# Optimization experiments

Measured on AMD Instinct MI355X. Metric: run time of the kernel, lower is better.

## Reference

```python
import jax, jax.numpy as jnp
import numpy as np

N = 131072       # total nodes (B graphs x P nodes)
P = 4096         # nodes per graph
B = 32           # graphs in batch
E = 2097152      # edges (avg degree 16)
IN_DIM = 64
HID = 128
OUT = 16
EPS = 1e-5
SLOPE = 0.01


def _degrees(idx):
    # structural degree, clamped to min 1 (as DGL GraphConv does)
    d = jax.ops.segment_sum(jnp.ones((E,), jnp.float32), idx, num_segments=N)
    return jnp.maximum(d, 1.0)


def _graph_conv(x, W, src, dst, ew):
    # DGL GraphConv, norm='both', bias=False, with scalar edge weights:
    # h = D_out^{-1/2} x ; m_v = sum_{(u->v)} w_e h_u ; out = (D_in^{-1/2} m) W
    h = x * jax.lax.rsqrt(_degrees(src))[:, None]
    m = jax.ops.segment_sum(ew[:, None] * h[src], dst, num_segments=N)  # [N, F]
    return (m * jax.lax.rsqrt(_degrees(dst))[:, None]) @ W


def _graph_norm(x, gamma, beta, alpha):
    # GraphNorm (Cai et al. / PyG, batch=None): stats over all nodes per feature
    mu = jnp.mean(x, axis=0)
    c = x - alpha * mu
    var = jnp.mean(c * c, axis=0)
    return c * jax.lax.rsqrt(var + EPS) * gamma + beta


def _mean_nodes(h, gid):
    # per-graph mean readout; every graph has exactly P nodes
    return jax.ops.segment_sum(h, gid, num_segments=B) / P


def setup_inputs() -> dict:
    key = jax.random.key(0)
    ks = jax.random.split(key, 8)
    src = jax.random.randint(ks[0], (E,), 0, N, dtype=jnp.int32)
    # keep edges within each 4096-node graph block (batched DGL graph)
    dst = (src // P) * P + jax.random.randint(ks[1], (E,), 0, P, dtype=jnp.int32)
    features = jax.random.normal(ks[2], (N, IN_DIM), jnp.float32)
    edge_weights = jax.random.uniform(ks[3], (E,), jnp.float32)
    # kaiming/xavier-scale init approximations
    W1 = jax.random.normal(ks[4], (IN_DIM, HID), jnp.float32) * np.sqrt(2.0 / IN_DIM)
    W2 = jax.random.normal(ks[5], (HID, HID), jnp.float32) * np.sqrt(2.0 / HID)
    Wc = jax.random.normal(ks[6], (OUT, 2 * HID), jnp.float32) * np.sqrt(1.0 / (2 * HID))
    ones = jnp.ones((HID,), jnp.float32)
    zeros = jnp.zeros((HID,), jnp.float32)
    return {
        'features': features, 'edge_weights': edge_weights, 'src': src, 'dst': dst,
        'W1': W1, 'W2': W2, 'Wc': Wc,
        'gamma1': ones, 'beta1': zeros, 'alpha1': ones,
        'gamma2': ones, 'beta2': zeros, 'alpha2': ones,
    }


def reference(features, edge_weights, src, dst, W1, W2, Wc,
              gamma1, beta1, alpha1, gamma2, beta2, alpha2):
    gid = jnp.arange(N, dtype=jnp.int32) // P  # node -> graph id
    h1 = _graph_conv(features, W1, src, dst, edge_weights)
    h1 = jax.nn.leaky_relu(_graph_norm(h1, gamma1, beta1, alpha1), SLOPE)
    r1 = _mean_nodes(h1, gid)                  # [B, HID]
    h2 = _graph_conv(h1, W2, src, dst, edge_weights)
    h2 = jax.nn.leaky_relu(_graph_norm(h2, gamma2, beta2, alpha2), SLOPE)
    r2 = _mean_nodes(h2, gid)                  # [B, HID]
    readouts = jnp.concatenate([r1, r2], axis=1)  # [B, 2*HID]
    return readouts @ Wc.T                     # [B, OUT]
```

## Files before the change

### kernel.cpp

```cpp
#include <hip/hip_runtime.h>
#include <hip/hip_fp16.h>

constexpr int NN   = 131072;
constexpr int PP   = 4096;
constexpr int BG   = 32;
constexpr int EE   = 2097152;
constexpr int IND  = 64;
constexpr int HH   = 128;
constexpr int CAP  = 81920;
constexpr float EPSV   = 1e-5f;
constexpr float SLOPEV = 0.01f;

typedef short bf16x8 __attribute__((ext_vector_type(8)));
typedef float f32x4  __attribute__((ext_vector_type(4)));
typedef float f32x2  __attribute__((ext_vector_type(2)));

__device__ __forceinline__ unsigned f2bf(float f) {
    unsigned u = __float_as_uint(f);
    return (u + 0x7FFFu + ((u >> 16) & 1u)) >> 16;
}
__device__ __forceinline__ unsigned pack2bf(float lo, float hi) {
    return f2bf(lo) | (f2bf(hi) << 16);
}
__device__ __forceinline__ float bflo(unsigned p) { return __uint_as_float(p << 16); }
__device__ __forceinline__ float bfhi(unsigned p) { return __uint_as_float(p & 0xFFFF0000u); }
__device__ __forceinline__ float w16(unsigned r) {
    return __half2float(__ushort_as_half((unsigned short)(r >> 16)));
}

template <int K>
__device__ __forceinline__ void packw_body(const float* __restrict__ W,
                                           unsigned short* __restrict__ pw, int t) {
    if (t >= K * 16) return;
    int lane = t & 63, nt = (t >> 6) & 7, kt = t >> 9;
    int kbase = kt * 32 + ((lane >> 4) & 3) * 8;
    int col   = nt * 16 + (lane & 15);
    for (int j = 0; j < 8; j++)
        pw[t * 8 + j] = (unsigned short)f2bf(W[(kbase + j) * HH + col]);
}

__global__ __launch_bounds__(256) void k_prep(const float* __restrict__ features,
                                              unsigned* __restrict__ f8x,
                                              const float* __restrict__ W1,
                                              unsigned short* __restrict__ pw1,
                                              const float* __restrict__ W2,
                                              unsigned short* __restrict__ pw2,
                                              int* __restrict__ gcur,
                                              float* __restrict__ racc,
                                              unsigned* __restrict__ csr2) {
    int b = blockIdx.x, t = threadIdx.x;
    if (b < 8192) {
        int i = b * 256 + t;
        float4 v = ((const float4*)features)[i];
        int w0 = __builtin_amdgcn_cvt_pk_fp8_f32(v.x, v.y, 0, false);
        int w1 = __builtin_amdgcn_cvt_pk_fp8_f32(v.z, v.w, w0, true);
        f8x[i] = (unsigned)w1;
        return;
    }
    if (b == 8192) {
        if (t < BG) gcur[t * 16] = t * CAP;
        for (int i = t; i < 2 * BG * HH; i += 256) racc[i] = 0.f;
        return;
    }
    if (b < 8197) { packw_body<64>(W1, pw1, (b - 8193) * 256 + t); return; }
    if (b < 8205) { packw_body<128>(W2, pw2, (b - 8197) * 256 + t); return; }
    ((uint4*)csr2)[(b - 8205) * 256 + t] = make_uint4(0, 0, 0, 0);
}

__global__ __launch_bounds__(256) void k_part(const int* __restrict__ src,
                                              const int* __restrict__ dst,
                                              const float* __restrict__ ew,
                                              int* __restrict__ gcur,
                                              uint2* __restrict__ recs) {
    __shared__ int cnt[32];
    __shared__ int start[32];
    __shared__ int gbase[32];
    __shared__ uint2 stage[4096];
    int t = threadIdx.x;
    int ebase = blockIdx.x * 4096;
    if (t < 32) cnt[t] = 0;
    __syncthreads();
    int es[16]; int ed[16]; float ev[16];
#pragma unroll
    for (int k = 0; k < 16; k++) {
        int e = ebase + k * 256 + t;
        es[k] = src[e]; ed[k] = dst[e]; ev[k] = ew[e];
        atomicAdd(&cnt[es[k] >> 12], 1);
    }
    __syncthreads();
    if (t == 0) {
        int run = 0;
        for (int g = 0; g < 32; g++) { start[g] = run; run += cnt[g]; }
    }
    __syncthreads();
    if (t < 32) {
        gbase[t] = atomicAdd(&gcur[t * 16], cnt[t]);
        cnt[t] = start[t];
    }
    __syncthreads();
#pragma unroll
    for (int k = 0; k < 16; k++) {
        int g = es[k] >> 12;
        int pos = atomicAdd(&cnt[g], 1);
        stage[pos] = make_uint2((unsigned)(es[k] & 4095) | ((unsigned)(ed[k] & 4095) << 12) |
                                ((unsigned)g << 24), __float_as_uint(ev[k]));
    }
    __syncthreads();
    for (int i = t; i < 4096; i += 256) {
        uint2 r = stage[i];
        int g = r.x >> 24;
        recs[gbase[g] + (i - start[g])] = r;
    }
}

__global__ __launch_bounds__(1024) void k_hist(const uint2* __restrict__ recs,
                                               const int* __restrict__ gcur,
                                               int* __restrict__ shist,
                                               int* __restrict__ dhist) {
    __shared__ int hs[4096];
    __shared__ int hd[4096];
    int t = threadIdx.x;
    int g = blockIdx.x >> 3, c = blockIdx.x & 7;
    int n = gcur[g * 16] - g * CAP;
    int lo = (n * c) >> 3, hi = (n * (c + 1)) >> 3;
    ((int4*)hs)[t] = make_int4(0, 0, 0, 0);
    ((int4*)hd)[t] = make_int4(0, 0, 0, 0);
    __syncthreads();
    const uint2* base = recs + (size_t)g * CAP;
    for (int i = lo + t; i < hi; i += 1024) {
        unsigned x = base[i].x;
        atomicAdd(&hs[x & 4095], 1);
        atomicAdd(&hd[(x >> 12) & 4095], 1);
    }
    __syncthreads();
    ((int4*)(shist + (size_t)blockIdx.x * 4096))[t] = ((int4*)hs)[t];
    ((int4*)(dhist + (size_t)blockIdx.x * 4096))[t] = ((int4*)hd)[t];
}

__global__ __launch_bounds__(1024) void k_offs(int* __restrict__ shist,
                                               int* __restrict__ dhist,
                                               float* __restrict__ rs_s,
                                               float* __restrict__ rsd,
                                               int* __restrict__ degd,
                                               int* __restrict__ offs) {
    __shared__ int partial[1024];
    int t = threadIdx.x, g = blockIdx.x;
    int sdeg[4] = {0, 0, 0, 0}, ddeg[4] = {0, 0, 0, 0};
#pragma unroll
    for (int c = 0; c < 8; c++) {
        int4 sv = ((const int4*)(shist + (size_t)(g * 8 + c) * 4096))[t];
        int4 dv = ((const int4*)(dhist + (size_t)(g * 8 + c) * 4096))[t];
        sdeg[0] += sv.x; sdeg[1] += sv.y; sdeg[2] += sv.z; sdeg[3] += sv.w;
        ddeg[0] += dv.x; ddeg[1] += dv.y; ddeg[2] += dv.z; ddeg[3] += dv.w;
    }
    int pdeg[4];
#pragma unroll
    for (int j = 0; j < 4; j++) {
        int idx = t * 4 + j;
        int vs = sdeg[j]; if (vs < 1) vs = 1;
        rs_s[g * PP + idx] = rsqrtf((float)vs);
        int vd = ddeg[j]; if (vd < 1) vd = 1;
        rsd[g * PP + idx]  = rsqrtf((float)vd);
        pdeg[j] = (ddeg[j] + 3) & ~3;
        degd[g * PP + idx] = pdeg[j];
    }
    partial[t] = pdeg[0] + pdeg[1] + pdeg[2] + pdeg[3];
    __syncthreads();
    for (int off = 1; off < 1024; off <<= 1) {
        int v = partial[t];
        int add = (t >= off) ? partial[t - off] : 0;
        __syncthreads();
        partial[t] = v + add;
        __syncthreads();
    }
    int run = (t == 0) ? 0 : partial[t - 1];
#pragma unroll
    for (int j = 0; j < 4; j++) {
        int idx = t * 4 + j;
        offs[g * PP + idx] = g * CAP + run;
        int nb = run;
        for (int c = 0; c < 8; c++) {
            size_t hidx = (size_t)(g * 8 + c) * 4096 + idx;
            int v = dhist[hidx];
            dhist[hidx] = nb;
            nb += v;
        }
        run += pdeg[j];
    }
}

__global__ __launch_bounds__(1024) void k_place(const uint2* __restrict__ recs,
                                                const int* __restrict__ gcur,
                                                const int* __restrict__ dhist,
                                                const float* __restrict__ rs_s,
                                                unsigned* __restrict__ csr2) {
    __shared__ int cur[4096];
    __shared__ float rss[4096];
    int t = threadIdx.x;
    int g = blockIdx.x >> 3, c = blockIdx.x & 7;
    int n = gcur[g * 16] - g * CAP;
    int lo = (n * c) >> 3, hi = (n * (c + 1)) >> 3;
    ((int4*)cur)[t] = ((const int4*)(dhist + (size_t)blockIdx.x * 4096))[t];
    ((float4*)rss)[t] = ((const float4*)(rs_s + (size_t)g * PP))[t];
    __syncthreads();
    const uint2* base = recs + (size_t)g * CAP;
    unsigned* cbase = csr2 + (size_t)g * CAP;
    for (int i = lo + t; i < hi; i += 1024) {
        uint2 r = base[i];
        int sl = r.x & 4095, dl = (r.x >> 12) & 4095;
        int pos = atomicAdd(&cur[dl], 1);
        float wf = __uint_as_float(r.y) * rss[sl];
        cbase[pos] = (unsigned)sl | ((unsigned)__half_as_ushort(__float2half(wf)) << 16);
    }
}

__device__ __forceinline__ void eacc2(unsigned rec, uint2 q,
                                      f32x2& P01, f32x2& P23, f32x2& P45, f32x2& P67) {
    f32x2 l0 = __builtin_amdgcn_cvt_pk_f32_fp8((int)q.x, false);
    f32x2 h0 = __builtin_amdgcn_cvt_pk_f32_fp8((int)q.x, true);
    f32x2 l1 = __builtin_amdgcn_cvt_pk_f32_fp8((int)q.y, false);
    f32x2 h1 = __builtin_amdgcn_cvt_pk_f32_fp8((int)q.y, true);
    float w = w16(rec);
    P01 += l0 * w; P23 += h0 * w; P45 += l1 * w; P67 += h1 * w;
}

template <int RW2>
__device__ __forceinline__ void agg_dual_w(const uint2* __restrict__ hp,
                                           const unsigned* __restrict__ csr2,
                                           int oa, int ca, int ob, int cb,
                                           f32x2& A01, f32x2& A23, f32x2& A45, f32x2& A67,
                                           f32x2& B01, f32x2& B23, f32x2& B45, f32x2& B67) {
    f32x2 z = {0.f, 0.f};
    A01 = z; A23 = z; A45 = z; A67 = z;
    B01 = z; B23 = z; B45 = z; B67 = z;
    int c0 = ca < cb ? ca : cb;
    int cm = ca < cb ? cb : ca;
    int i = 0;
    for (; i < c0; i += 4) {
        uint4 ra = *(const uint4*)(csr2 + oa + i);
        uint4 rb = *(const uint4*)(csr2 + ob + i);
        uint2 qa0 = hp[(ra.x & 4095u) * RW2];
        uint2 qa1 = hp[(ra.y & 4095u) * RW2];
        uint2 qa2 = hp[(ra.z & 4095u) * RW2];
        uint2 qa3 = hp[(ra.w & 4095u) * RW2];
        uint2 qb0 = hp[(rb.x & 4095u) * RW2];
        uint2 qb1 = hp[(rb.y & 4095u) * RW2];
        uint2 qb2 = hp[(rb.z & 4095u) * RW2];
        uint2 qb3 = hp[(rb.w & 4095u) * RW2];
        eacc2(ra.x, qa0, A01, A23, A45, A67);
        eacc2(ra.y, qa1, A01, A23, A45, A67);
        eacc2(ra.z, qa2, A01, A23, A45, A67);
        eacc2(ra.w, qa3, A01, A23, A45, A67);
        eacc2(rb.x, qb0, B01, B23, B45, B67);
        eacc2(rb.y, qb1, B01, B23, B45, B67);
        eacc2(rb.z, qb2, B01, B23, B45, B67);
        eacc2(rb.w, qb3, B01, B23, B45, B67);
    }
    if (i < cm) {
        int ot = (ca > cb) ? oa : ob;
        f32x2 E01 = z, E23 = z, E45 = z, E67 = z;
        for (; i < cm; i += 4) {
            uint4 rr = *(const uint4*)(csr2 + ot + i);
            uint2 q0 = hp[(rr.x & 4095u) * RW2];
            uint2 q1 = hp[(rr.y & 4095u) * RW2];
            uint2 q2 = hp[(rr.z & 4095u) * RW2];
            uint2 q3 = hp[(rr.w & 4095u) * RW2];
            eacc2(rr.x, q0, E01, E23, E45, E67);
            eacc2(rr.y, q1, E01, E23, E45, E67);
            eacc2(rr.z, q2, E01, E23, E45, E67);
            eacc2(rr.w, q3, E01, E23, E45, E67);
        }
        if (ca > cb) { A01 += E01; A23 += E23; A45 += E45; A67 += E67; }
        else         { B01 += E01; B23 += E23; B45 += E45; B67 += E67; }
    }
}

__global__ __launch_bounds__(256) void k_aggemm1(const unsigned* __restrict__ f8x,
                                                 const unsigned* __restrict__ csr2,
                                                 const int* __restrict__ offs,
                                                 const int* __restrict__ degd,
                                                 const float* __restrict__ rsd,
                                                 const short* __restrict__ PW,
                                                 unsigned short* __restrict__ C,
                                                 float* __restrict__ part) {
    constexpr int WP = 36;
    __shared__ unsigned lds[64 * WP];
    __shared__ float s1[HH], s2[HH];
    int t = threadIdx.x;
    if (t < HH) { s1[t] = 0.f; s2[t] = 0.f; }
    int bid = blockIdx.x;
    int xcd = bid & 7, idx = bid >> 3;
    int g = xcd * 4 + (idx >> 6);
    int node0 = g * PP + (idx & 63) * 64;
    int lane = t & 63, wv = t >> 6;
    int grp = lane >> 3, gl = lane & 7;
    const uint2* hp = (const uint2*)f8x + (size_t)((unsigned)(g * PP)) * 8 + gl;
    {
        int lrA = wv * 16 + grp * 2;
        int va = node0 + lrA;
        int2 oo = *(const int2*)(offs + va);
        int2 dd = *(const int2*)(degd + va);
        f32x2 A01, A23, A45, A67, B01, B23, B45, B67;
        agg_dual_w<8>(hp, csr2, oo.x, dd.x, oo.y, dd.y,
                      A01, A23, A45, A67, B01, B23, B45, B67);
        float2 rr2 = *(const float2*)(rsd + va);
        *(uint4*)&lds[lrA * WP + gl * 4] = make_uint4(
            pack2bf(A01.x * rr2.x, A01.y * rr2.x), pack2bf(A23.x * rr2.x, A23.y * rr2.x),
            pack2bf(A45.x * rr2.x, A45.y * rr2.x), pack2bf(A67.x * rr2.x, A67.y * rr2.x));
        *(uint4*)&lds[(lrA + 1) * WP + gl * 4] = make_uint4(
            pack2bf(B01.x * rr2.y, B01.y * rr2.y), pack2bf(B23.x * rr2.y, B23.y * rr2.y),
            pack2bf(B45.x * rr2.y, B45.y * rr2.y), pack2bf(B67.x * rr2.y, B67.y * rr2.y));
    }
    __syncthreads();
    int m = lane & 15, quad = lane >> 4;
    bf16x8 a[2];
#pragma unroll
    for (int kt = 0; kt < 2; kt++)
        a[kt] = *(const bf16x8*)&lds[(wv * 16 + m) * WP + kt * 16 + quad * 4];
#pragma unroll
    for (int nt = 0; nt < 8; nt++) {
        f32x4 acc = {0.f, 0.f, 0.f, 0.f};
#pragma unroll
        for (int kt = 0; kt < 2; kt++) {
            bf16x8 b = *(const bf16x8*)(PW + ((size_t)(kt * 8 + nt) * 64 + lane) * 8);
            acc = __builtin_amdgcn_mfma_f32_16x16x32_bf16(a[kt], b, acc, 0, 0, 0);
        }
        int col = nt * 16 + m;
        int r0 = node0 + wv * 16 + quad * 4;
        float ps = 0.f, pq = 0.f;
#pragma unroll
        for (int r = 0; r < 4; r++) {
            C[(size_t)(r0 + r) * HH + col] = (unsigned short)f2bf(acc[r]);
            ps += acc[r]; pq += acc[r] * acc[r];
        }
        atomicAdd(&s1[col], ps);
        atomicAdd(&s2[col], pq);
    }
    __syncthreads();
    if (t < HH) {
        part[bid * 256 + t]      = s1[t];
        part[bid * 256 + HH + t] = s2[t];
    }
}

__global__ __launch_bounds__(256) void k_aggemm2(const unsigned* __restrict__ f8,
                                                 const unsigned* __restrict__ csr2,
                                                 const int* __restrict__ offs,
                                                 const int* __restrict__ degd,
                                                 const float* __restrict__ rsd,
                                                 const short* __restrict__ PW,
                                                 unsigned short* __restrict__ C,
                                                 float* __restrict__ part) {
    constexpr int WP = 68;
    __shared__ unsigned lds[64 * WP];
    __shared__ float s1[HH], s2[HH];
    int t = threadIdx.x;
    if (t < HH) { s1[t] = 0.f; s2[t] = 0.f; }
    int bid = blockIdx.x;
    int xcd = bid & 7, idx = bid >> 3;
    int g = xcd * 4 + (idx >> 6);
    int node0 = g * PP + (idx & 63) * 64;
    int lane = t & 63, wv = t >> 6;
    int grp = lane >> 4, gl = lane & 15;
    const uint2* hp = (const uint2*)f8 + (size_t)((unsigned)(g * PP)) * 16 + gl;
    for (int p = 0; p < 2; p++) {
        int lrA = wv * 16 + p * 8 + grp * 2;
        int va = node0 + lrA;
        int2 oo = *(const int2*)(offs + va);
        int2 dd = *(const int2*)(degd + va);
        f32x2 A01, A23, A45, A67, B01, B23, B45, B67;
        agg_dual_w<16>(hp, csr2, oo.x, dd.x, oo.y, dd.y,
                       A01, A23, A45, A67, B01, B23, B45, B67);
        float2 rr2 = *(const float2*)(rsd + va);
        *(uint4*)&lds[lrA * WP + gl * 4] = make_uint4(
            pack2bf(A01.x * rr2.x, A01.y * rr2.x), pack2bf(A23.x * rr2.x, A23.y * rr2.x),
            pack2bf(A45.x * rr2.x, A45.y * rr2.x), pack2bf(A67.x * rr2.x, A67.y * rr2.x));
        *(uint4*)&lds[(lrA + 1) * WP + gl * 4] = make_uint4(
            pack2bf(B01.x * rr2.y, B01.y * rr2.y), pack2bf(B23.x * rr2.y, B23.y * rr2.y),
            pack2bf(B45.x * rr2.y, B45.y * rr2.y), pack2bf(B67.x * rr2.y, B67.y * rr2.y));
    }
    __syncthreads();
    int m = lane & 15, quad = lane >> 4;
    bf16x8 a[4];
#pragma unroll
    for (int kt = 0; kt < 4; kt++)
        a[kt] = *(const bf16x8*)&lds[(wv * 16 + m) * WP + kt * 16 + quad * 4];
#pragma unroll
    for (int nt = 0; nt < 8; nt++) {
        f32x4 acc = {0.f, 0.f, 0.f, 0.f};
#pragma unroll
        for (int kt = 0; kt < 4; kt++) {
            bf16x8 b = *(const bf16x8*)(PW + ((size_t)(kt * 8 + nt) * 64 + lane) * 8);
            acc = __builtin_amdgcn_mfma_f32_16x16x32_bf16(a[kt], b, acc, 0, 0, 0);
        }
        int col = nt * 16 + m;
        int r0 = node0 + wv * 16 + quad * 4;
        float ps = 0.f, pq = 0.f;
#pragma unroll
        for (int r = 0; r < 4; r++) {
            C[(size_t)(r0 + r) * HH + col] = (unsigned short)f2bf(acc[r]);
            ps += acc[r]; pq += acc[r] * acc[r];
        }
        atomicAdd(&s1[col], ps);
        atomicAdd(&s2[col], pq);
    }
    __syncthreads();
    if (t < HH) {
        part[bid * 256 + t]      = s1[t];
        part[bid * 256 + HH + t] = s2[t];
    }
}

__global__ __launch_bounds__(256) void k_red(const float* __restrict__ part,
                                             float* __restrict__ pb) {
    int t = threadIdx.x, b = blockIdx.x;
    float s = 0.f;
    for (int r = 0; r < 32; r++) s += part[(size_t)(b * 32 + r) * 256 + t];
    pb[b * 256 + t] = s;
}

__global__ void k_coef(const float* __restrict__ pb, const float* __restrict__ gamma,
                       const float* __restrict__ beta, const float* __restrict__ alpha,
                       float* __restrict__ ab) {
    int t = threadIdx.x;
    float s = 0.f;
    for (int b = 0; b < 64; b++) s += pb[b * 256 + t];
    __shared__ float sh[256];
    sh[t] = s;
    __syncthreads();
    if (t < 128) {
        float mu = sh[t] * (1.f / NN);
        float e2 = sh[128 + t] * (1.f / NN);
        float al = alpha[t];
        float var = e2 - (2.f * al - al * al) * mu * mu;
        float a = rsqrtf(var + EPSV) * gamma[t];
        ab[t] = a;
        ab[HH + t] = beta[t] - al * mu * a;
    }
}

template <bool WRITE>
__global__ __launch_bounds__(256) void k_normro(const unsigned* __restrict__ h,
                                                const float* __restrict__ ab,
                                                float* __restrict__ racc,
                                                unsigned short* __restrict__ f8) {
    int fp = threadIdx.x & 63;
    int q  = threadIdx.x >> 6;
    int node0 = blockIdx.x * 64;
    int g = node0 / PP;
    float a0 = ab[2 * fp], a1 = ab[2 * fp + 1];
    float b0 = ab[HH + 2 * fp], b1 = ab[HH + 2 * fp + 1];
    float s0 = 0.f, s1 = 0.f;
    for (int i = q; i < 64; i += 4) {
        size_t idx = (size_t)(node0 + i) * 64 + fp;
        unsigned v = h[idx];
        float x0 = fmaf(a0, bflo(v), b0); x0 = x0 > 0.f ? x0 : SLOPEV * x0;
        float x1 = fmaf(a1, bfhi(v), b1); x1 = x1 > 0.f ? x1 : SLOPEV * x1;
        if (WRITE) f8[idx] = (unsigned short)__builtin_amdgcn_cvt_pk_fp8_f32(x0, x1, 0, false);
        s0 += x0; s1 += x1;
    }
    __shared__ float sh[512];
    sh[threadIdx.x] = s0;
    sh[256 + threadIdx.x] = s1;
    __syncthreads();
    if (q == 0) {
        float t0 = s0 + sh[64 + fp] + sh[128 + fp] + sh[192 + fp];
        float t1 = s1 + sh[256 + 64 + fp] + sh[256 + 128 + fp] + sh[256 + 192 + fp];
        atomicAdd(&racc[g * HH + 2 * fp],     t0);
        atomicAdd(&racc[g * HH + 2 * fp + 1], t1);
    }
}

__global__ void k_final(const float* __restrict__ racc1, const float* __restrict__ racc2,
                        const float* __restrict__ Wc, float* __restrict__ out) {
    int t = threadIdx.x;
    int b = t >> 4, o = t & 15;
    float acc = 0.f;
    for (int f = 0; f < HH; f++) acc += racc1[b * HH + f] * Wc[o * (2 * HH) + f];
    for (int f = 0; f < HH; f++) acc += racc2[b * HH + f] * Wc[o * (2 * HH) + HH + f];
    out[t] = acc * (1.f / PP);
}

extern "C" void kernel_launch(void* const* d_in, const int* in_sizes, int n_in,
                              void* d_out, int out_size, void* d_ws, size_t ws_size,
                              hipStream_t stream) {
    const float* features = (const float*)d_in[0];
    const float* ew       = (const float*)d_in[1];
    const int*   src      = (const int*)d_in[2];
    const int*   dst      = (const int*)d_in[3];
    const float* W1       = (const float*)d_in[4];
    const float* W2       = (const float*)d_in[5];
    const float* Wc       = (const float*)d_in[6];
    const float* gamma1   = (const float*)d_in[7];
    const float* beta1    = (const float*)d_in[8];
    const float* alpha1   = (const float*)d_in[9];
    const float* gamma2   = (const float*)d_in[10];
    const float* beta2    = (const float*)d_in[11];
    const float* alpha2   = (const float*)d_in[12];
    float* out = (float*)d_out;

    char* w = (char*)d_ws;
    int*    gcur   = (int*)(w + 0);
    float*  racc1  = (float*)(w + (16u << 10));
    float*  racc2  = (float*)(w + (32u << 10));
    float*  ab1    = (float*)(w + (48u << 10));
    float*  ab2    = (float*)(w + (52u << 10));
    unsigned short* pw1 = (unsigned short*)(w + (64u << 10));
    unsigned short* pw2 = (unsigned short*)(w + (80u << 10));
    float*  pb     = (float*)(w + (128u << 10));
    float*  rs_s   = (float*)(w + (1024u << 10));
    float*  rsd    = (float*)(w + (1536u << 10));
    int*    degd   = (int*)(w + (2048u << 10));
    int*    offs   = (int*)(w + (2560u << 10));
    float*  part   = (float*)(w + (3u << 20));
    int*    shist  = (int*)(w + (5u << 20));
    int*    dhist  = (int*)(w + (9u << 20));
    unsigned* csr2 = (unsigned*)(w + (13u << 20));
    unsigned* mbuf = (unsigned*)(w + (23u << 20));
    unsigned* hbuf = (unsigned*)(w + (55u << 20));
    uint2*    recs = (uint2*)(w + (87u << 20));
    unsigned* f8x  = (unsigned*)(w + (107u << 20));
    unsigned* f8buf= (unsigned*)(w + (123u << 20));

    k_prep<<<10765, 256, 0, stream>>>(features, f8x, W1, pw1, W2, pw2, gcur, racc1, csr2);

    k_part<<<EE / 4096, 256, 0, stream>>>(src, dst, ew, gcur, recs);
    k_hist<<<BG * 8, 1024, 0, stream>>>(recs, gcur, shist, dhist);
    k_offs<<<BG, 1024, 0, stream>>>(shist, dhist, rs_s, rsd, degd, offs);
    k_place<<<BG * 8, 1024, 0, stream>>>(recs, gcur, dhist, rs_s, csr2);

    k_aggemm1<<<NN / 64, 256, 0, stream>>>(f8x, csr2, offs, degd, rsd,
                                           (const short*)pw1, (unsigned short*)hbuf, part);
    k_red<<<64, 256, 0, stream>>>(part, pb);
    k_coef<<<1, 256, 0, stream>>>(pb, gamma1, beta1, alpha1, ab1);
    k_normro<true><<<NN / 64, 256, 0, stream>>>(hbuf, ab1, racc1, (unsigned short*)f8buf);

    k_aggemm2<<<NN / 64, 256, 0, stream>>>(f8buf, csr2, offs, degd, rsd,
                                           (const short*)pw2, (unsigned short*)mbuf, part);
    k_red<<<64, 256, 0, stream>>>(part, pb);
    k_coef<<<1, 256, 0, stream>>>(pb, gamma2, beta2, alpha2, ab2);
    k_normro<false><<<NN / 64, 256, 0, stream>>>(mbuf, ab2, racc2, nullptr);

    k_final<<<1, 512, 0, stream>>>(racc1, racc2, Wc, out);
}
```

Measured before the change: 358.9 us.

## Build CSR directly with global atomics, dropping graph-partition and histogram passes

Replaces the four-kernel CSR build (partition edges by graph into records, per-chunk LDS histograms, scan, LDS-cursor placement) with three kernels. Degrees now come from global atomics straight off src/dst, a per-graph scan produces offsets and cursors, and edges are placed using global atomics on those cursors. This removes the intermediate record buffer and one full pass over edges, but it moves all counting and cursor atomics from LDS to global memory. The rs_s gather is also now random. The workspace zeroing grows to clear the new degree arrays.

```diff
diff --git a/kernel.cpp b/kernel.cpp
--- a/kernel.cpp
+++ b/kernel.cpp
@@ -45,7 +45,7 @@
                                               unsigned short* __restrict__ pw1,
                                               const float* __restrict__ W2,
                                               unsigned short* __restrict__ pw2,
-                                              int* __restrict__ gcur,
+                                              int* __restrict__ degz,
                                               float* __restrict__ racc,
                                               unsigned* __restrict__ csr2) {
     int b = blockIdx.x, t = threadIdx.x;
@@ -58,111 +58,58 @@
         return;
     }
     if (b == 8192) {
-        if (t < BG) gcur[t * 16] = t * CAP;
         for (int i = t; i < 2 * BG * HH; i += 256) racc[i] = 0.f;
         return;
     }
     if (b < 8197) { packw_body<64>(W1, pw1, (b - 8193) * 256 + t); return; }
     if (b < 8205) { packw_body<128>(W2, pw2, (b - 8197) * 256 + t); return; }
-    ((uint4*)csr2)[(b - 8205) * 256 + t] = make_uint4(0, 0, 0, 0);
-}
-
-__global__ __launch_bounds__(256) void k_part(const int* __restrict__ src,
-                                              const int* __restrict__ dst,
-                                              const float* __restrict__ ew,
-                                              int* __restrict__ gcur,
-                                              uint2* __restrict__ recs) {
-    __shared__ int cnt[32];
-    __shared__ int start[32];
-    __shared__ int gbase[32];
-    __shared__ uint2 stage[4096];
-    int t = threadIdx.x;
-    int ebase = blockIdx.x * 4096;
-    if (t < 32) cnt[t] = 0;
-    __syncthreads();
-    int es[16]; int ed[16]; float ev[16];
-#pragma unroll
-    for (int k = 0; k < 16; k++) {
-        int e = ebase + k * 256 + t;
-        es[k] = src[e]; ed[k] = dst[e]; ev[k] = ew[e];
-        atomicAdd(&cnt[es[k] >> 12], 1);
-    }
-    __syncthreads();
-    if (t == 0) {
-        int run = 0;
-        for (int g = 0; g < 32; g++) { start[g] = run; run += cnt[g]; }
-    }
-    __syncthreads();
-    if (t < 32) {
-        gbase[t] = atomicAdd(&gcur[t * 16], cnt[t]);
-        cnt[t] = start[t];
-    }
-    __syncthreads();
-#pragma unroll
-    for (int k = 0; k < 16; k++) {
-        int g = es[k] >> 12;
-        int pos = atomicAdd(&cnt[g], 1);
-        stage[pos] = make_uint2((unsigned)(es[k] & 4095) | ((unsigned)(ed[k] & 4095) << 12) |
-                                ((unsigned)g << 24), __float_as_uint(ev[k]));
-    }
-    __syncthreads();
-    for (int i = t; i < 4096; i += 256) {
-        uint2 r = stage[i];
-        int g = r.x >> 24;
-        recs[gbase[g] + (i - start[g])] = r;
-    }
-}
-
-__global__ __launch_bounds__(1024) void k_hist(const uint2* __restrict__ recs,
-                                               const int* __restrict__ gcur,
-                                               int* __restrict__ shist,
-                                               int* __restrict__ dhist) {
-    __shared__ int hs[4096];
-    __shared__ int hd[4096];
-    int t = threadIdx.x;
-    int g = blockIdx.x >> 3, c = blockIdx.x & 7;
-    int n = gcur[g * 16] - g * CAP;
-    int lo = (n * c) >> 3, hi = (n * (c + 1)) >> 3;
-    ((int4*)hs)[t] = make_int4(0, 0, 0, 0);
-    ((int4*)hd)[t] = make_int4(0, 0, 0, 0);
-    __syncthreads();
-    const uint2* base = recs + (size_t)g * CAP;
-    for (int i = lo + t; i < hi; i += 1024) {
-        unsigned x = base[i].x;
-        atomicAdd(&hs[x & 4095], 1);
-        atomicAdd(&hd[(x >> 12) & 4095], 1);
-    }
-    __syncthreads();
-    ((int4*)(shist + (size_t)blockIdx.x * 4096))[t] = ((int4*)hs)[t];
-    ((int4*)(dhist + (size_t)blockIdx.x * 4096))[t] = ((int4*)hd)[t];
-}
-
-__global__ __launch_bounds__(1024) void k_offs(int* __restrict__ shist,
-                                               int* __restrict__ dhist,
+    if (b < 10765) {
+        ((uint4*)csr2)[(b - 8205) * 256 + t] = make_uint4(0, 0, 0, 0);
+        return;
+    }
+    ((uint4*)degz)[(b - 10765) * 256 + t] = make_uint4(0, 0, 0, 0);
+}
+
+__global__ __launch_bounds__(256) void k_deg(const int* __restrict__ src,
+                                             const int* __restrict__ dst,
+                                             int* __restrict__ sdeg,
+                                             int* __restrict__ ddeg) {
+    int e0 = blockIdx.x * 2048 + threadIdx.x * 8;
+    int4 sa = *(const int4*)(src + e0), sb = *(const int4*)(src + e0 + 4);
+    int4 da = *(const int4*)(dst + e0), db = *(const int4*)(dst + e0 + 4);
+    atomicAdd(&sdeg[sa.x], 1); atomicAdd(&sdeg[sa.y], 1);
+    atomicAdd(&sdeg[sa.z], 1); atomicAdd(&sdeg[sa.w], 1);
+    atomicAdd(&sdeg[sb.x], 1); atomicAdd(&sdeg[sb.y], 1);
+    atomicAdd(&sdeg[sb.z], 1); atomicAdd(&sdeg[sb.w], 1);
+    atomicAdd(&ddeg[da.x], 1); atomicAdd(&ddeg[da.y], 1);
+    atomicAdd(&ddeg[da.z], 1); atomicAdd(&ddeg[da.w], 1);
+    atomicAdd(&ddeg[db.x], 1); atomicAdd(&ddeg[db.y], 1);
+    atomicAdd(&ddeg[db.z], 1); atomicAdd(&ddeg[db.w], 1);
+}
+
+__global__ __launch_bounds__(1024) void k_scan(const int* __restrict__ sdeg,
+                                               const int* __restrict__ ddeg,
                                                float* __restrict__ rs_s,
                                                float* __restrict__ rsd,
                                                int* __restrict__ degd,
-                                               int* __restrict__ offs) {
+                                               int* __restrict__ offs,
+                                               int* __restrict__ cur) {
     __shared__ int partial[1024];
     int t = threadIdx.x, g = blockIdx.x;
-    int sdeg[4] = {0, 0, 0, 0}, ddeg[4] = {0, 0, 0, 0};
-#pragma unroll
-    for (int c = 0; c < 8; c++) {
-        int4 sv = ((const int4*)(shist + (size_t)(g * 8 + c) * 4096))[t];
-        int4 dv = ((const int4*)(dhist + (size_t)(g * 8 + c) * 4096))[t];
-        sdeg[0] += sv.x; sdeg[1] += sv.y; sdeg[2] += sv.z; sdeg[3] += sv.w;
-        ddeg[0] += dv.x; ddeg[1] += dv.y; ddeg[2] += dv.z; ddeg[3] += dv.w;
-    }
+    int base = g * PP + t * 4;
+    int4 sd = *(const int4*)(sdeg + base);
+    int4 dd = *(const int4*)(ddeg + base);
+    int s[4] = {sd.x, sd.y, sd.z, sd.w};
+    int d[4] = {dd.x, dd.y, dd.z, dd.w};
     int pdeg[4];
 #pragma unroll
     for (int j = 0; j < 4; j++) {
-        int idx = t * 4 + j;
-        int vs = sdeg[j]; if (vs < 1) vs = 1;
-        rs_s[g * PP + idx] = rsqrtf((float)vs);
-        int vd = ddeg[j]; if (vd < 1) vd = 1;
-        rsd[g * PP + idx]  = rsqrtf((float)vd);
-        pdeg[j] = (ddeg[j] + 3) & ~3;
-        degd[g * PP + idx] = pdeg[j];
+        int vs = s[j] < 1 ? 1 : s[j];
+        rs_s[base + j] = rsqrtf((float)vs);
+        int vd = d[j] < 1 ? 1 : d[j];
+        rsd[base + j] = rsqrtf((float)vd);
+        pdeg[j] = (d[j] + 3) & ~3;
+        degd[base + j] = pdeg[j];
     }
     partial[t] = pdeg[0] + pdeg[1] + pdeg[2] + pdeg[3];
     __syncthreads();
@@ -176,41 +123,31 @@
     int run = (t == 0) ? 0 : partial[t - 1];
 #pragma unroll
     for (int j = 0; j < 4; j++) {
-        int idx = t * 4 + j;
-        offs[g * PP + idx] = g * CAP + run;
-        int nb = run;
-        for (int c = 0; c < 8; c++) {
-            size_t hidx = (size_t)(g * 8 + c) * 4096 + idx;
-            int v = dhist[hidx];
-            dhist[hidx] = nb;
-            nb += v;
-        }
+        offs[base + j] = g * CAP + run;
+        cur[base + j]  = g * CAP + run;
         run += pdeg[j];
     }
 }
 
-__global__ __launch_bounds__(1024) void k_place(const uint2* __restrict__ recs,
-                                                const int* __restrict__ gcur,
-                                                const int* __restrict__ dhist,
+__global__ __launch_bounds__(256) void k_place2(const int* __restrict__ src,
+                                                const int* __restrict__ dst,
+                                                const float* __restrict__ ew,
                                                 const float* __restrict__ rs_s,
+                                                int* __restrict__ cur,
                                                 unsigned* __restrict__ csr2) {
-    __shared__ int cur[4096];
-    __shared__ float rss[4096];
-    int t = threadIdx.x;
-    int g = blockIdx.x >> 3, c = blockIdx.x & 7;
-    int n = gcur[g * 16] - g * CAP;
-    int lo = (n * c) >> 3, hi = (n * (c + 1)) >> 3;
-    ((int4*)cur)[t] = ((const int4*)(dhist + (size_t)blockIdx.x * 4096))[t];
-    ((float4*)rss)[t] = ((const float4*)(rs_s + (size_t)g * PP))[t];
-    __syncthreads();
-    const uint2* base = recs + (size_t)g * CAP;
-    unsigned* cbase = csr2 + (size_t)g * CAP;
-    for (int i = lo + t; i < hi; i += 1024) {
-        uint2 r = base[i];
-        int sl = r.x & 4095, dl = (r.x >> 12) & 4095;
-        int pos = atomicAdd(&cur[dl], 1);
-        float wf = __uint_as_float(r.y) * rss[sl];
-        cbase[pos] = (unsigned)sl | ((unsigned)__half_as_ushort(__float2half(wf)) << 16);
+    int e0 = blockIdx.x * 2048 + threadIdx.x * 8;
+    int4 sa = *(const int4*)(src + e0), sb = *(const int4*)(src + e0 + 4);
+    int4 da = *(const int4*)(dst + e0), db = *(const int4*)(dst + e0 + 4);
+    float4 wa = *(const float4*)(ew + e0), wb = *(const float4*)(ew + e0 + 4);
+    int ss[8] = {sa.x, sa.y, sa.z, sa.w, sb.x, sb.y, sb.z, sb.w};
+    int ds[8] = {da.x, da.y, da.z, da.w, db.x, db.y, db.z, db.w};
+    float ws[8] = {wa.x, wa.y, wa.z, wa.w, wb.x, wb.y, wb.z, wb.w};
+#pragma unroll
+    for (int k = 0; k < 8; k++) {
+        float wf = ws[k] * rs_s[ss[k]];
+        int pos = atomicAdd(&cur[ds[k]], 1);
+        csr2[pos] = (unsigned)(ss[k] & 4095) |
+                    ((unsigned)__half_as_ushort(__float2half(wf)) << 16);
     }
 }
 
@@ -500,7 +437,6 @@
     float* out = (float*)d_out;
 
     char* w = (char*)d_ws;
-    int*    gcur   = (int*)(w + 0);
     float*  racc1  = (float*)(w + (16u << 10));
     float*  racc2  = (float*)(w + (32u << 10));
     float*  ab1    = (float*)(w + (48u << 10));
@@ -513,21 +449,20 @@
     int*    degd   = (int*)(w + (2048u << 10));
     int*    offs   = (int*)(w + (2560u << 10));
     float*  part   = (float*)(w + (3u << 20));
-    int*    shist  = (int*)(w + (5u << 20));
-    int*    dhist  = (int*)(w + (9u << 20));
+    int*    sdeg   = (int*)(w + (5u << 20));
+    int*    ddeg   = (int*)(w + (5u << 20) + (512u << 10));
+    int*    cur    = (int*)(w + (9u << 20));
     unsigned* csr2 = (unsigned*)(w + (13u << 20));
     unsigned* mbuf = (unsigned*)(w + (23u << 20));
     unsigned* hbuf = (unsigned*)(w + (55u << 20));
-    uint2*    recs = (uint2*)(w + (87u << 20));
     unsigned* f8x  = (unsigned*)(w + (107u << 20));
     unsigned* f8buf= (unsigned*)(w + (123u << 20));
 
-    k_prep<<<10765, 256, 0, stream>>>(features, f8x, W1, pw1, W2, pw2, gcur, racc1, csr2);
-
-    k_part<<<EE / 4096, 256, 0, stream>>>(src, dst, ew, gcur, recs);
-    k_hist<<<BG * 8, 1024, 0, stream>>>(recs, gcur, shist, dhist);
-    k_offs<<<BG, 1024, 0, stream>>>(shist, dhist, rs_s, rsd, degd, offs);
-    k_place<<<BG * 8, 1024, 0, stream>>>(recs, gcur, dhist, rs_s, csr2);
+    k_prep<<<11021, 256, 0, stream>>>(features, f8x, W1, pw1, W2, pw2, sdeg, racc1, csr2);
+
+    k_deg<<<EE / 2048, 256, 0, stream>>>(src, dst, sdeg, ddeg);
+    k_scan<<<BG, 1024, 0, stream>>>(sdeg, ddeg, rs_s, rsd, degd, offs, cur);
+    k_place2<<<EE / 2048, 256, 0, stream>>>(src, dst, ew, rs_s, cur, csr2);
 
     k_aggemm1<<<NN / 64, 256, 0, stream>>>(f8x, csr2, offs, degd, rsd,
                                            (const short*)pw1, (unsigned short*)hbuf, part);
```

Measured after the change: 561.2 us. 1.56x slower.

## Double aggemm threads per node block and fuse stat reduction kernels

Applied to the files above, without the earlier changes.

Both aggregation+GEMM kernels move from 256 to 512 threads per block. In layer 1 each 8-lane group now handles a single node instead of two. In layer 2 the per-thread loop over two passes is removed. The MFMA stage splits its eight column tiles across two wave halves. Separately, the two-kernel stat reduction (k_red then k_coef) is merged into one kernel that uses a last-block atomic counter to compute the norm coefficients, saving a launch per layer. The cost is extra threadfence and atomic overhead, plus doubled per-block register and thread demand.

```diff
diff --git a/kernel.cpp b/kernel.cpp
--- a/kernel.cpp
+++ b/kernel.cpp
@@ -47,7 +47,8 @@
                                               unsigned short* __restrict__ pw2,
                                               int* __restrict__ gcur,
                                               float* __restrict__ racc,
-                                              unsigned* __restrict__ csr2) {
+                                              unsigned* __restrict__ csr2,
+                                              int* __restrict__ scnt) {
     int b = blockIdx.x, t = threadIdx.x;
     if (b < 8192) {
         int i = b * 256 + t;
@@ -59,6 +60,7 @@
     }
     if (b == 8192) {
         if (t < BG) gcur[t * 16] = t * CAP;
+        if (t == 0) scnt[0] = 0;
         for (int i = t; i < 2 * BG * HH; i += 256) racc[i] = 0.f;
         return;
     }
@@ -275,7 +277,27 @@
     }
 }
 
-__global__ __launch_bounds__(256) void k_aggemm1(const unsigned* __restrict__ f8x,
+template <int RW2>
+__device__ __forceinline__ void agg_single_w(const uint2* __restrict__ hp,
+                                             const unsigned* __restrict__ csr2,
+                                             int oa, int ca,
+                                             f32x2& A01, f32x2& A23, f32x2& A45, f32x2& A67) {
+    f32x2 z = {0.f, 0.f};
+    A01 = z; A23 = z; A45 = z; A67 = z;
+    for (int i = 0; i < ca; i += 4) {
+        uint4 ra = *(const uint4*)(csr2 + oa + i);
+        uint2 q0 = hp[(ra.x & 4095u) * RW2];
+        uint2 q1 = hp[(ra.y & 4095u) * RW2];
+        uint2 q2 = hp[(ra.z & 4095u) * RW2];
+        uint2 q3 = hp[(ra.w & 4095u) * RW2];
+        eacc2(ra.x, q0, A01, A23, A45, A67);
+        eacc2(ra.y, q1, A01, A23, A45, A67);
+        eacc2(ra.z, q2, A01, A23, A45, A67);
+        eacc2(ra.w, q3, A01, A23, A45, A67);
+    }
+}
+
+__global__ __launch_bounds__(512) void k_aggemm1(const unsigned* __restrict__ f8x,
                                                  const unsigned* __restrict__ csr2,
                                                  const int* __restrict__ offs,
                                                  const int* __restrict__ degd,
@@ -292,33 +314,29 @@
     int xcd = bid & 7, idx = bid >> 3;
     int g = xcd * 4 + (idx >> 6);
     int node0 = g * PP + (idx & 63) * 64;
-    int lane = t & 63, wv = t >> 6;
-    int grp = lane >> 3, gl = lane & 7;
+    int gr = t >> 3, gl = t & 7;
     const uint2* hp = (const uint2*)f8x + (size_t)((unsigned)(g * PP)) * 8 + gl;
     {
-        int lrA = wv * 16 + grp * 2;
-        int va = node0 + lrA;
-        int2 oo = *(const int2*)(offs + va);
-        int2 dd = *(const int2*)(degd + va);
-        f32x2 A01, A23, A45, A67, B01, B23, B45, B67;
-        agg_dual_w<8>(hp, csr2, oo.x, dd.x, oo.y, dd.y,
-                      A01, A23, A45, A67, B01, B23, B45, B67);
-        float2 rr2 = *(const float2*)(rsd + va);
-        *(uint4*)&lds[lrA * WP + gl * 4] = make_uint4(
-            pack2bf(A01.x * rr2.x, A01.y * rr2.x), pack2bf(A23.x * rr2.x, A23.y * rr2.x),
-            pack2bf(A45.x * rr2.x, A45.y * rr2.x), pack2bf(A67.x * rr2.x, A67.y * rr2.x));
-        *(uint4*)&lds[(lrA + 1) * WP + gl * 4] = make_uint4(
-            pack2bf(B01.x * rr2.y, B01.y * rr2.y), pack2bf(B23.x * rr2.y, B23.y * rr2.y),
-            pack2bf(B45.x * rr2.y, B45.y * rr2.y), pack2bf(B67.x * rr2.y, B67.y * rr2.y));
-    }
-    __syncthreads();
+        int va = node0 + gr;
+        int oa = offs[va], ca = degd[va];
+        f32x2 A01, A23, A45, A67;
+        agg_single_w<8>(hp, csr2, oa, ca, A01, A23, A45, A67);
+        float rda = rsd[va];
+        *(uint4*)&lds[gr * WP + gl * 4] = make_uint4(
+            pack2bf(A01.x * rda, A01.y * rda), pack2bf(A23.x * rda, A23.y * rda),
+            pack2bf(A45.x * rda, A45.y * rda), pack2bf(A67.x * rda, A67.y * rda));
+    }
+    __syncthreads();
+    int lane = t & 63, wv = t >> 6;
+    int rowblk = wv & 3, colh = wv >> 2;
     int m = lane & 15, quad = lane >> 4;
     bf16x8 a[2];
 #pragma unroll
     for (int kt = 0; kt < 2; kt++)
-        a[kt] = *(const bf16x8*)&lds[(wv * 16 + m) * WP + kt * 16 + quad * 4];
-#pragma unroll
-    for (int nt = 0; nt < 8; nt++) {
+        a[kt] = *(const bf16x8*)&lds[(rowblk * 16 + m) * WP + kt * 16 + quad * 4];
+#pragma unroll
+    for (int nq = 0; nq < 4; nq++) {
+        int nt = colh * 4 + nq;
         f32x4 acc = {0.f, 0.f, 0.f, 0.f};
 #pragma unroll
         for (int kt = 0; kt < 2; kt++) {
@@ -326,7 +344,7 @@
             acc = __builtin_amdgcn_mfma_f32_16x16x32_bf16(a[kt], b, acc, 0, 0, 0);
         }
         int col = nt * 16 + m;
-        int r0 = node0 + wv * 16 + quad * 4;
+        int r0 = node0 + rowblk * 16 + quad * 4;
         float ps = 0.f, pq = 0.f;
 #pragma unroll
         for (int r = 0; r < 4; r++) {
@@ -343,7 +361,7 @@
     }
 }
 
-__global__ __launch_bounds__(256) void k_aggemm2(const unsigned* __restrict__ f8,
+__global__ __launch_bounds__(512) void k_aggemm2(const unsigned* __restrict__ f8,
                                                  const unsigned* __restrict__ csr2,
                                                  const int* __restrict__ offs,
                                                  const int* __restrict__ degd,
@@ -360,11 +378,10 @@
     int xcd = bid & 7, idx = bid >> 3;
     int g = xcd * 4 + (idx >> 6);
     int node0 = g * PP + (idx & 63) * 64;
-    int lane = t & 63, wv = t >> 6;
-    int grp = lane >> 4, gl = lane & 15;
+    int gr = t >> 4, gl = t & 15;
     const uint2* hp = (const uint2*)f8 + (size_t)((unsigned)(g * PP)) * 16 + gl;
-    for (int p = 0; p < 2; p++) {
-        int lrA = wv * 16 + p * 8 + grp * 2;
+    {
+        int lrA = gr * 2;
         int va = node0 + lrA;
         int2 oo = *(const int2*)(offs + va);
         int2 dd = *(const int2*)(degd + va);
@@ -380,13 +397,16 @@
             pack2bf(B45.x * rr2.y, B45.y * rr2.y), pack2bf(B67.x * rr2.y, B67.y * rr2.y));
     }
     __syncthreads();
+    int lane = t & 63, wv = t >> 6;
+    int rowblk = wv & 3, colh = wv >> 2;
     int m = lane & 15, quad = lane >> 4;
     bf16x8 a[4];
 #pragma unroll
     for (int kt = 0; kt < 4; kt++)
-        a[kt] = *(const bf16x8*)&lds[(wv * 16 + m) * WP + kt * 16 + quad * 4];
-#pragma unroll
-    for (int nt = 0; nt < 8; nt++) {
+        a[kt] = *(const bf16x8*)&lds[(rowblk * 16 + m) * WP + kt * 16 + quad * 4];
+#pragma unroll
+    for (int nq = 0; nq < 4; nq++) {
+        int nt = colh * 4 + nq;
         f32x4 acc = {0.f, 0.f, 0.f, 0.f};
 #pragma unroll
         for (int kt = 0; kt < 4; kt++) {
@@ -394,7 +414,7 @@
             acc = __builtin_amdgcn_mfma_f32_16x16x32_bf16(a[kt], b, acc, 0, 0, 0);
         }
         int col = nt * 16 + m;
-        int r0 = node0 + wv * 16 + quad * 4;
+        int r0 = node0 + rowblk * 16 + quad * 4;
         float ps = 0.f, pq = 0.f;
 #pragma unroll
         for (int r = 0; r < 4; r++) {
@@ -411,22 +431,27 @@
     }
 }
 
-__global__ __launch_bounds__(256) void k_red(const float* __restrict__ part,
-                                             float* __restrict__ pb) {
+__global__ __launch_bounds__(256) void k_stat(const float* __restrict__ part,
+                                              const float* __restrict__ gamma,
+                                              const float* __restrict__ beta,
+                                              const float* __restrict__ alpha,
+                                              float* __restrict__ ab,
+                                              float* __restrict__ pb,
+                                              int* __restrict__ scnt) {
     int t = threadIdx.x, b = blockIdx.x;
     float s = 0.f;
     for (int r = 0; r < 32; r++) s += part[(size_t)(b * 32 + r) * 256 + t];
     pb[b * 256 + t] = s;
-}
-
-__global__ void k_coef(const float* __restrict__ pb, const float* __restrict__ gamma,
-                       const float* __restrict__ beta, const float* __restrict__ alpha,
-                       float* __restrict__ ab) {
-    int t = threadIdx.x;
-    float s = 0.f;
-    for (int b = 0; b < 64; b++) s += pb[b * 256 + t];
+    __threadfence();
+    __shared__ int isLast;
+    if (t == 0) isLast = (atomicAdd(scnt, 1) == 63) ? 1 : 0;
+    __syncthreads();
+    if (!isLast) return;
+    __threadfence();
+    float tot = 0.f;
+    for (int bb = 0; bb < 64; bb++) tot += pb[bb * 256 + t];
     __shared__ float sh[256];
-    sh[t] = s;
+    sh[t] = tot;
     __syncthreads();
     if (t < 128) {
         float mu = sh[t] * (1.f / NN);
@@ -437,6 +462,7 @@
         ab[t] = a;
         ab[HH + t] = beta[t] - al * mu * a;
     }
+    if (t == 0) scnt[0] = 0;
 }
 
 template <bool WRITE>
@@ -505,6 +531,7 @@
     float*  racc2  = (float*)(w + (32u << 10));
     float*  ab1    = (float*)(w + (48u << 10));
     float*  ab2    = (float*)(w + (52u << 10));
+    int*    scnt   = (int*)(w + (56u << 10));
     unsigned short* pw1 = (unsigned short*)(w + (64u << 10));
     unsigned short* pw2 = (unsigned short*)(w + (80u << 10));
     float*  pb     = (float*)(w + (128u << 10));
@@ -522,23 +549,21 @@
     unsigned* f8x  = (unsigned*)(w + (107u << 20));
     unsigned* f8buf= (unsigned*)(w + (123u << 20));
 
-    k_prep<<<10765, 256, 0, stream>>>(features, f8x, W1, pw1, W2, pw2, gcur, racc1, csr2);
+    k_prep<<<10765, 256, 0, stream>>>(features, f8x, W1, pw1, W2, pw2, gcur, racc1, csr2, scnt);
 
     k_part<<<EE / 4096, 256, 0, stream>>>(src, dst, ew, gcur, recs);
     k_hist<<<BG * 8, 1024, 0, stream>>>(recs, gcur, shist, dhist);
     k_offs<<<BG, 1024, 0, stream>>>(shist, dhist, rs_s, rsd, degd, offs);
     k_place<<<BG * 8, 1024, 0, stream>>>(recs, gcur, dhist, rs_s, csr2);
 
-    k_aggemm1<<<NN / 64, 256, 0, stream>>>(f8x, csr2, offs, degd, rsd,
+    k_aggemm1<<<NN / 64, 512, 0, stream>>>(f8x, csr2, offs, degd, rsd,
                                            (const short*)pw1, (unsigned short*)hbuf, part);
-    k_red<<<64, 256, 0, stream>>>(part, pb);
-    k_coef<<<1, 256, 0, stream>>>(pb, gamma1, beta1, alpha1, ab1);
+    k_stat<<<64, 256, 0, stream>>>(part, gamma1, beta1, alpha1, ab1, pb, scnt);
     k_normro<true><<<NN / 64, 256, 0, stream>>>(hbuf, ab1, racc1, (unsigned short*)f8buf);
 
-    k_aggemm2<<<NN / 64, 256, 0, stream>>>(f8buf, csr2, offs, degd, rsd,
+    k_aggemm2<<<NN / 64, 512, 0, stream>>>(f8buf, csr2, offs, degd, rsd,
                                            (const short*)pw2, (unsigned short*)mbuf, part);
-    k_red<<<64, 256, 0, stream>>>(part, pb);
-    k_coef<<<1, 256, 0, stream>>>(pb, gamma2, beta2, alpha2, ab2);
+    k_stat<<<64, 256, 0, stream>>>(part, gamma2, beta2, alpha2, ab2, pb, scnt);
     k_normro<false><<<NN / 64, 256, 0, stream>>>(mbuf, ab2, racc2, nullptr);
 
     k_final<<<1, 512, 0, stream>>>(racc1, racc2, Wc, out);
```

Result: slower. 369.1 us (+2.8%).
